# Kernel optimization log

Hardware: AMD Instinct MI355X
Metric: run time of the kernel (lower is better)

## Reference

```python
import jax, jax.numpy as jnp
import numpy as np

TAU = 0.2
EPS_NORM = 1e-12  # torch F.normalize eps


def _l2_normalize(x):
    n = jnp.linalg.norm(x, axis=-1, keepdims=True)
    return x / jnp.maximum(n, EPS_NORM)


def setup_inputs() -> dict:
    key = jax.random.key(0)
    k1, k2 = jax.random.split(key)
    seg_emb = jax.random.normal(k1, (131072, 512), dtype=jnp.float32)
    prototypes = jax.random.normal(k2, (64, 512), dtype=jnp.float32) * 0.02
    return {"seg_emb": seg_emb, "prototypes": prototypes}


def reference(seg_emb, prototypes):
    # normalize -> cosine-sim matmul -> temperature scale -> softmax -> weighted proto sum
    p = _l2_normalize(prototypes)          # [K, D]
    z = _l2_normalize(seg_emb)             # [N, D]
    logits = jnp.einsum('nd,kd->nk', z, p) / max(TAU, 1e-06)  # [N, K]
    w = jax.nn.softmax(logits, axis=-1)    # [N, K]
    pattern = jnp.einsum('nk,kd->nd', w, prototypes)           # [N, D]
    return pattern, w, logits
```

## Files before the change

kernel.cpp:

```cpp
#include <hip/hip_runtime.h>
#include <hip/hip_bf16.h>

typedef __attribute__((ext_vector_type(8))) short short8;
typedef __attribute__((ext_vector_type(4))) float f32x4;

#define NPROTO 64
#define DIM    512
#define TAU_INV 5.0f

__device__ __forceinline__ unsigned short f2bf(float f) {
    union { float f; unsigned int u; } v; v.f = f;
    unsigned int r = v.u + 0x7FFFu + ((v.u >> 16) & 1u);
    return (unsigned short)(r >> 16);
}

__global__ void pb_prep(const float* __restrict__ protos,
                        unsigned short* __restrict__ pnorm,
                        unsigned short* __restrict__ protosT) {
    const int k    = blockIdx.x;
    const int lane = threadIdx.x;
    const float* row = protos + k * DIM;
    float x[8];
    float ss = 0.0f;
#pragma unroll
    for (int j = 0; j < 8; ++j) {
        x[j] = row[lane * 8 + j];
        ss += x[j] * x[j];
    }
#pragma unroll
    for (int m = 1; m < 64; m <<= 1) ss += __shfl_xor(ss, m, 64);
    const float s = 1.0f / fmaxf(sqrtf(ss), 1e-12f);
    short8 pn;
#pragma unroll
    for (int j = 0; j < 8; ++j) pn[j] = (short)f2bf(x[j] * s);
    *reinterpret_cast<short8*>(pnorm + k * DIM + lane * 8) = pn;
#pragma unroll
    for (int j = 0; j < 8; ++j)
        protosT[(lane * 8 + j) * NPROTO + k] = f2bf(x[j]);
}

__global__ __launch_bounds__(256, 2) void pb_main(
    const float* __restrict__ seg,
    const unsigned short* __restrict__ pnorm,
    const unsigned short* __restrict__ protosT,
    float* __restrict__ out_pat,
    float* __restrict__ out_w,
    float* __restrict__ out_log) {

    __shared__ char bufA[4 * 4 * 4096];
    __shared__ unsigned short wbuf_all[4 * 2 * 16 * 64];

    const int wid  = (int)(threadIdx.x >> 6);
    const int lane = (int)(threadIdx.x & 63);
    const int g    = lane >> 4;
    const int r16  = lane & 15;
    const long n0  = ((long)blockIdx.x * 4 + wid) * 32;

    const int sr = lane >> 3;
    const int sj = (lane & 7) ^ (sr & 7);
    const float* sbase = seg + (n0 + sr) * DIM + sj * 4;
    char* wavebuf = bufA + wid * 4096;

#define STAGE(KT) do {                                                         \
    char* _d = wavebuf + ((KT) & 3) * 16384;                                   \
    const float* _s = sbase + (KT) * 32;                                       \
    _Pragma("unroll")                                                          \
    for (int _i = 0; _i < 4; ++_i)                                             \
        __builtin_amdgcn_global_load_lds(                                      \
            (const __attribute__((address_space(1))) void*)(_s + _i * 8 * DIM),\
            (__attribute__((address_space(3))) void*)(_d + _i * 1024),         \
            16, 0, 0);                                                         \
} while (0)

    short8 breg[4][4];
#define BLOAD(KT) do {                                                         \
    _Pragma("unroll")                                                          \
    for (int _c = 0; _c < 4; ++_c)                                             \
        breg[(KT) & 3][_c] = *reinterpret_cast<const short8*>(                 \
            pnorm + (_c * 16 + r16) * DIM + g * 8 + (KT) * 32);                \
} while (0)

    f32x4 acc0[4] = {}, acc1[4] = {};
    float ss0 = 0.0f, ss1 = 0.0f;

    STAGE(0); BLOAD(0);
    STAGE(1); BLOAD(1);
    STAGE(2); BLOAD(2);

    const int ra  = r16 & 7;
    const int s0a = ((2 * g)     ^ ra) * 16;
    const int s0b = ((2 * g + 1) ^ ra) * 16;

#pragma unroll
    for (int kt = 0; kt < 16; ++kt) {
        if (kt + 3 < 16) { STAGE(kt + 3); BLOAD(kt + 3); }
        if (kt <= 12)      asm volatile("s_waitcnt vmcnt(24)" ::: "memory");
        else if (kt == 13) asm volatile("s_waitcnt vmcnt(16)" ::: "memory");
        else if (kt == 14) asm volatile("s_waitcnt vmcnt(8)"  ::: "memory");
        else               asm volatile("s_waitcnt vmcnt(0)"  ::: "memory");
        __builtin_amdgcn_sched_barrier(0);

        char* sb = wavebuf + (kt & 3) * 16384;
        const f32x4 a00 = *reinterpret_cast<const f32x4*>(sb + r16 * 128 + s0a);
        const f32x4 a01 = *reinterpret_cast<const f32x4*>(sb + r16 * 128 + s0b);
        const f32x4 a10 = *reinterpret_cast<const f32x4*>(sb + (16 + r16) * 128 + s0a);
        const f32x4 a11 = *reinterpret_cast<const f32x4*>(sb + (16 + r16) * 128 + s0b);

        short8 af0, af1;
#pragma unroll
        for (int j = 0; j < 4; ++j) {
            ss0 += a00[j] * a00[j] + a01[j] * a01[j];
            ss1 += a10[j] * a10[j] + a11[j] * a11[j];
            af0[j] = (short)f2bf(a00[j]); af0[j + 4] = (short)f2bf(a01[j]);
            af1[j] = (short)f2bf(a10[j]); af1[j + 4] = (short)f2bf(a11[j]);
        }
#pragma unroll
        for (int c = 0; c < 4; ++c) {
            acc0[c] = __builtin_amdgcn_mfma_f32_16x16x32_bf16(af0, breg[kt & 3][c], acc0[c], 0, 0, 0);
            acc1[c] = __builtin_amdgcn_mfma_f32_16x16x32_bf16(af1, breg[kt & 3][c], acc1[c], 0, 0, 0);
        }
    }

    ss0 += __shfl_xor(ss0, 16, 64); ss0 += __shfl_xor(ss0, 32, 64);
    ss1 += __shfl_xor(ss1, 16, 64); ss1 += __shfl_xor(ss1, 32, 64);
    const float sco0 = TAU_INV / fmaxf(sqrtf(ss0), 1e-12f);
    const float sco1 = TAU_INV / fmaxf(sqrtf(ss1), 1e-12f);
    float sc0[4], sc1[4];
#pragma unroll
    for (int q = 0; q < 4; ++q) {
        sc0[q] = __shfl(sco0, g * 4 + q, 64);
        sc1[q] = __shfl(sco1, g * 4 + q, 64);
    }

    float lg0[4][4], lg1[4][4];
#pragma unroll
    for (int c = 0; c < 4; ++c)
#pragma unroll
        for (int q = 0; q < 4; ++q) {
            lg0[c][q] = acc0[c][q] * sc0[q];
            lg1[c][q] = acc1[c][q] * sc1[q];
            out_log[(n0 + g * 4 + q) * NPROTO + c * 16 + r16]      = lg0[c][q];
            out_log[(n0 + 16 + g * 4 + q) * NPROTO + c * 16 + r16] = lg1[c][q];
        }

    float w0[4][4], w1[4][4];
#pragma unroll
    for (int q = 0; q < 4; ++q) {
        float mx0 = fmaxf(fmaxf(lg0[0][q], lg0[1][q]), fmaxf(lg0[2][q], lg0[3][q]));
        float mx1 = fmaxf(fmaxf(lg1[0][q], lg1[1][q]), fmaxf(lg1[2][q], lg1[3][q]));
#pragma unroll
        for (int msk = 1; msk < 16; msk <<= 1) {
            mx0 = fmaxf(mx0, __shfl_xor(mx0, msk, 64));
            mx1 = fmaxf(mx1, __shfl_xor(mx1, msk, 64));
        }
        float e0[4], e1[4], sum0 = 0.0f, sum1 = 0.0f;
#pragma unroll
        for (int c = 0; c < 4; ++c) {
            e0[c] = __expf(lg0[c][q] - mx0); sum0 += e0[c];
            e1[c] = __expf(lg1[c][q] - mx1); sum1 += e1[c];
        }
#pragma unroll
        for (int msk = 1; msk < 16; msk <<= 1) {
            sum0 += __shfl_xor(sum0, msk, 64);
            sum1 += __shfl_xor(sum1, msk, 64);
        }
        const float i0 = 1.0f / sum0, i1 = 1.0f / sum1;
#pragma unroll
        for (int c = 0; c < 4; ++c) { w0[c][q] = e0[c] * i0; w1[c][q] = e1[c] * i1; }
    }

    unsigned short* wb0 = wbuf_all + (wid * 2 + 0) * (16 * 64);
    unsigned short* wb1 = wbuf_all + (wid * 2 + 1) * (16 * 64);
#pragma unroll
    for (int c = 0; c < 4; ++c)
#pragma unroll
        for (int q = 0; q < 4; ++q) {
            out_w[(n0 + g * 4 + q) * NPROTO + c * 16 + r16]      = w0[c][q];
            out_w[(n0 + 16 + g * 4 + q) * NPROTO + c * 16 + r16] = w1[c][q];
            const int row  = g * 4 + q;
            const int col  = c * 16 + r16;
            const int byte = (row * 128 + col * 2) ^ ((row & 7) << 4);
            *reinterpret_cast<unsigned short*>(reinterpret_cast<char*>(wb0) + byte) = f2bf(w0[c][q]);
            *reinterpret_cast<unsigned short*>(reinterpret_cast<char*>(wb1) + byte) = f2bf(w1[c][q]);
        }

    __syncthreads();

    short8 wa[2][2];
    {
        const int row = r16;
        const int b0 = (row * 128 + g * 16)      ^ ((row & 7) << 4);
        const int b1 = (row * 128 + g * 16 + 64) ^ ((row & 7) << 4);
        wa[0][0] = *reinterpret_cast<const short8*>(reinterpret_cast<char*>(wb0) + b0);
        wa[0][1] = *reinterpret_cast<const short8*>(reinterpret_cast<char*>(wb0) + b1);
        wa[1][0] = *reinterpret_cast<const short8*>(reinterpret_cast<char*>(wb1) + b0);
        wa[1][1] = *reinterpret_cast<const short8*>(reinterpret_cast<char*>(wb1) + b1);
    }

    short8 pbuf[2][2];
    const unsigned short* btile = protosT + r16 * NPROTO + g * 8;
    pbuf[0][0] = *reinterpret_cast<const short8*>(btile);
    pbuf[0][1] = *reinterpret_cast<const short8*>(btile + 32);
#pragma unroll
    for (int cp = 0; cp < 32; ++cp) {
        if (cp < 31) {
            const unsigned short* bn = btile + (cp + 1) * 16 * NPROTO;
            pbuf[(cp + 1) & 1][0] = *reinterpret_cast<const short8*>(bn);
            pbuf[(cp + 1) & 1][1] = *reinterpret_cast<const short8*>(bn + 32);
        }
        f32x4 p0 = {}, p1 = {};
        p0 = __builtin_amdgcn_mfma_f32_16x16x32_bf16(wa[0][0], pbuf[cp & 1][0], p0, 0, 0, 0);
        p0 = __builtin_amdgcn_mfma_f32_16x16x32_bf16(wa[0][1], pbuf[cp & 1][1], p0, 0, 0, 0);
        p1 = __builtin_amdgcn_mfma_f32_16x16x32_bf16(wa[1][0], pbuf[cp & 1][0], p1, 0, 0, 0);
        p1 = __builtin_amdgcn_mfma_f32_16x16x32_bf16(wa[1][1], pbuf[cp & 1][1], p1, 0, 0, 0);
#pragma unroll
        for (int q = 0; q < 4; ++q) {
            out_pat[(n0 + g * 4 + q) * DIM + cp * 16 + r16]      = p0[q];
            out_pat[(n0 + 16 + g * 4 + q) * DIM + cp * 16 + r16] = p1[q];
        }
    }
#undef STAGE
#undef BLOAD
}

extern "C" void kernel_launch(void* const* d_in, const int* in_sizes, int n_in,
                              void* d_out, int out_size, void* d_ws, size_t ws_size,
                              hipStream_t stream) {
    const float* seg    = (const float*)d_in[0];
    const float* protos = (const float*)d_in[1];
    const int N = in_sizes[0] / DIM;

    float* out     = (float*)d_out;
    float* out_pat = out;
    float* out_w   = out_pat + (size_t)N * DIM;
    float* out_log = out_w + (size_t)N * NPROTO;

    unsigned short* pnorm   = (unsigned short*)d_ws;
    unsigned short* protosT = pnorm + NPROTO * DIM;

    pb_prep<<<NPROTO, 64, 0, stream>>>(protos, pnorm, protosT);
    pb_main<<<N / 128, 256, 0, stream>>>(seg, pnorm, protosT, out_pat, out_w, out_log);
}
```

Measured before the change: 169.2 us.

## Load seg tiles directly into registers instead of async LDS staging

Drops the global_load_lds staging of the fp32 seg tiles through shared memory and the hand-placed vmcnt waits. Each lane now loads its fragment straight from global into registers, with a 3-slot register ring for A and a 2-slot ring for the prototype B fragments. This frees 64KB of LDS, which may allow more resident blocks, and removes the LDS read step. In exchange it raises register pressure and leaves load waits to the compiler, so latency may be hidden less well.

```diff
diff --git a/kernel.cpp b/kernel.cpp
--- a/kernel.cpp
+++ b/kernel.cpp
@@ -47,7 +47,6 @@
     float* __restrict__ out_w,
     float* __restrict__ out_log) {
 
-    __shared__ char bufA[4 * 4 * 4096];
     __shared__ unsigned short wbuf_all[4 * 2 * 16 * 64];
 
     const int wid  = (int)(threadIdx.x >> 6);
@@ -56,70 +55,54 @@
     const int r16  = lane & 15;
     const long n0  = ((long)blockIdx.x * 4 + wid) * 32;
 
-    const int sr = lane >> 3;
-    const int sj = (lane & 7) ^ (sr & 7);
-    const float* sbase = seg + (n0 + sr) * DIM + sj * 4;
-    char* wavebuf = bufA + wid * 4096;
-
-#define STAGE(KT) do {                                                         \
-    char* _d = wavebuf + ((KT) & 3) * 16384;                                   \
-    const float* _s = sbase + (KT) * 32;                                       \
-    _Pragma("unroll")                                                          \
-    for (int _i = 0; _i < 4; ++_i)                                             \
-        __builtin_amdgcn_global_load_lds(                                      \
-            (const __attribute__((address_space(1))) void*)(_s + _i * 8 * DIM),\
-            (__attribute__((address_space(3))) void*)(_d + _i * 1024),         \
-            16, 0, 0);                                                         \
+    f32x4 acc0[4] = {}, acc1[4] = {};
+    float ss0 = 0.0f, ss1 = 0.0f;
+    const float* ap0 = seg + (n0 + r16) * DIM + g * 8;
+    const float* ap1 = ap0 + 16 * DIM;
+
+    f32x4 abuf[3][4];
+    short8 bbuf[2][4];
+
+#define ALOAD(SLOT, KT) do {                                                   \
+    abuf[SLOT][0] = *reinterpret_cast<const f32x4*>(ap0 + (KT) * 32);          \
+    abuf[SLOT][1] = *reinterpret_cast<const f32x4*>(ap0 + (KT) * 32 + 4);      \
+    abuf[SLOT][2] = *reinterpret_cast<const f32x4*>(ap1 + (KT) * 32);          \
+    abuf[SLOT][3] = *reinterpret_cast<const f32x4*>(ap1 + (KT) * 32 + 4);      \
 } while (0)
-
-    short8 breg[4][4];
-#define BLOAD(KT) do {                                                         \
+#define BLOAD(SLOT, KT) do {                                                   \
+    const unsigned short* _bb = pnorm + r16 * DIM + g * 8 + (KT) * 32;         \
     _Pragma("unroll")                                                          \
     for (int _c = 0; _c < 4; ++_c)                                             \
-        breg[(KT) & 3][_c] = *reinterpret_cast<const short8*>(                 \
-            pnorm + (_c * 16 + r16) * DIM + g * 8 + (KT) * 32);                \
+        bbuf[SLOT][_c] = *reinterpret_cast<const short8*>(_bb + _c * 16 * DIM);\
 } while (0)
 
-    f32x4 acc0[4] = {}, acc1[4] = {};
-    float ss0 = 0.0f, ss1 = 0.0f;
-
-    STAGE(0); BLOAD(0);
-    STAGE(1); BLOAD(1);
-    STAGE(2); BLOAD(2);
-
-    const int ra  = r16 & 7;
-    const int s0a = ((2 * g)     ^ ra) * 16;
-    const int s0b = ((2 * g + 1) ^ ra) * 16;
+    ALOAD(0, 0); ALOAD(1, 1);
+    BLOAD(0, 0);
 
 #pragma unroll
     for (int kt = 0; kt < 16; ++kt) {
-        if (kt + 3 < 16) { STAGE(kt + 3); BLOAD(kt + 3); }
-        if (kt <= 12)      asm volatile("s_waitcnt vmcnt(24)" ::: "memory");
-        else if (kt == 13) asm volatile("s_waitcnt vmcnt(16)" ::: "memory");
-        else if (kt == 14) asm volatile("s_waitcnt vmcnt(8)"  ::: "memory");
-        else               asm volatile("s_waitcnt vmcnt(0)"  ::: "memory");
-        __builtin_amdgcn_sched_barrier(0);
-
-        char* sb = wavebuf + (kt & 3) * 16384;
-        const f32x4 a00 = *reinterpret_cast<const f32x4*>(sb + r16 * 128 + s0a);
-        const f32x4 a01 = *reinterpret_cast<const f32x4*>(sb + r16 * 128 + s0b);
-        const f32x4 a10 = *reinterpret_cast<const f32x4*>(sb + (16 + r16) * 128 + s0a);
-        const f32x4 a11 = *reinterpret_cast<const f32x4*>(sb + (16 + r16) * 128 + s0b);
+        const int cur = kt % 3;
+        if (kt < 14) ALOAD((kt + 2) % 3, kt + 2);
+        if (kt < 15) BLOAD((kt + 1) & 1, kt + 1);
 
         short8 af0, af1;
 #pragma unroll
         for (int j = 0; j < 4; ++j) {
-            ss0 += a00[j] * a00[j] + a01[j] * a01[j];
-            ss1 += a10[j] * a10[j] + a11[j] * a11[j];
-            af0[j] = (short)f2bf(a00[j]); af0[j + 4] = (short)f2bf(a01[j]);
-            af1[j] = (short)f2bf(a10[j]); af1[j + 4] = (short)f2bf(a11[j]);
+            const float x00 = abuf[cur][0][j], x01 = abuf[cur][1][j];
+            const float x10 = abuf[cur][2][j], x11 = abuf[cur][3][j];
+            ss0 += x00 * x00 + x01 * x01;
+            ss1 += x10 * x10 + x11 * x11;
+            af0[j] = (short)f2bf(x00); af0[j + 4] = (short)f2bf(x01);
+            af1[j] = (short)f2bf(x10); af1[j + 4] = (short)f2bf(x11);
         }
 #pragma unroll
         for (int c = 0; c < 4; ++c) {
-            acc0[c] = __builtin_amdgcn_mfma_f32_16x16x32_bf16(af0, breg[kt & 3][c], acc0[c], 0, 0, 0);
-            acc1[c] = __builtin_amdgcn_mfma_f32_16x16x32_bf16(af1, breg[kt & 3][c], acc1[c], 0, 0, 0);
-        }
-    }
+            acc0[c] = __builtin_amdgcn_mfma_f32_16x16x32_bf16(af0, bbuf[kt & 1][c], acc0[c], 0, 0, 0);
+            acc1[c] = __builtin_amdgcn_mfma_f32_16x16x32_bf16(af1, bbuf[kt & 1][c], acc1[c], 0, 0, 0);
+        }
+    }
+#undef ALOAD
+#undef BLOAD
 
     ss0 += __shfl_xor(ss0, 16, 64); ss0 += __shfl_xor(ss0, 32, 64);
     ss1 += __shfl_xor(ss1, 16, 64); ss1 += __shfl_xor(ss1, 32, 64);
@@ -169,8 +152,8 @@
         for (int c = 0; c < 4; ++c) { w0[c][q] = e0[c] * i0; w1[c][q] = e1[c] * i1; }
     }
 
-    unsigned short* wb0 = wbuf_all + (wid * 2 + 0) * (16 * 64);
-    unsigned short* wb1 = wbuf_all + (wid * 2 + 1) * (16 * 64);
+    unsigned short* wb0 = wbuf_all + (wid * 2 + 0) * 1024;
+    unsigned short* wb1 = wbuf_all + (wid * 2 + 1) * 1024;
 #pragma unroll
     for (int c = 0; c < 4; ++c)
 #pragma unroll
@@ -188,9 +171,8 @@
 
     short8 wa[2][2];
     {
-        const int row = r16;
-        const int b0 = (row * 128 + g * 16)      ^ ((row & 7) << 4);
-        const int b1 = (row * 128 + g * 16 + 64) ^ ((row & 7) << 4);
+        const int b0 = (r16 * 128 + g * 16)      ^ ((r16 & 7) << 4);
+        const int b1 = (r16 * 128 + g * 16 + 64) ^ ((r16 & 7) << 4);
         wa[0][0] = *reinterpret_cast<const short8*>(reinterpret_cast<char*>(wb0) + b0);
         wa[0][1] = *reinterpret_cast<const short8*>(reinterpret_cast<char*>(wb0) + b1);
         wa[1][0] = *reinterpret_cast<const short8*>(reinterpret_cast<char*>(wb1) + b0);
@@ -219,8 +201,6 @@
             out_pat[(n0 + 16 + g * 4 + q) * DIM + cp * 16 + r16] = p1[q];
         }
     }
-#undef STAGE
-#undef BLOAD
 }
 
 extern "C" void kernel_launch(void* const* d_in, const int* in_sizes, int n_in,
```

Result: slower. 177.6 us (+5.0%).
